# Optimization experiments

Measured on AMD Instinct MI355X. Metric: run time of the kernel, lower is better.

Reference implementation:

```python
import jax, jax.numpy as jnp
import numpy as np

NUM_CLASSES = 80
SCORE_THR = 0.2
NMS_THR = 0.3
MAX_PER_IMAGE = 100
TOPK_PER_CLASS = 100  # cap on pre-NMS candidates per (image, class); >= max_per_image
ANCHOR_MASK = [[6, 7, 8], [3, 4, 5], [0, 1, 2]]
COCO_ANCHORS = np.array([[10, 13], [16, 30], [33, 23], [30, 61], [62, 45],
                         [59, 119], [116, 90], [156, 198], [373, 326]], dtype=np.float32)


def yolo_head(feats, layer_anchors, num_classes, input_shape):
    # feats: [B, 3*(5+C), gh, gw]
    B = feats.shape[0]
    gh, gw = feats.shape[2], feats.shape[3]
    na = layer_anchors.shape[0]
    f = feats.reshape(B, na, num_classes + 5, gh, gw).transpose(0, 3, 4, 1, 2)  # [B,gh,gw,3,5+C]
    gy, gx = jnp.meshgrid(jnp.arange(gh), jnp.arange(gw), indexing='ij')
    grid = jnp.stack([gx, gy], axis=-1).astype(f.dtype)[None, :, :, None, :]  # [1,gh,gw,1,2]
    # literal translation: divide by tensor([gh, gw]) (square grids in practice)
    box_xy = (jax.nn.sigmoid(f[..., :2]) + grid) / jnp.array([gh, gw], f.dtype)
    box_wh = jnp.exp(f[..., 2:4]) * layer_anchors[None, None, None, :, :] / input_shape[None, None, None, None, :]
    conf = jax.nn.sigmoid(f[..., 4:5])
    probs = jax.nn.sigmoid(f[..., 5:])
    return box_xy, box_wh, conf, probs


def yolo_correct_boxes(box_xy, box_wh, input_shape, image_shape):
    box_yx = box_xy[..., ::-1]
    box_hw = box_wh[..., ::-1]
    new_shape = jnp.round(image_shape * jnp.min(input_shape / image_shape))
    offset = (input_shape - new_shape) / 2.0 / input_shape
    scale = input_shape / new_shape
    box_yx = (box_yx - offset) * scale
    box_hw = box_hw * scale
    mins = box_yx - box_hw / 2.0
    maxes = box_yx + box_hw / 2.0
    boxes = jnp.concatenate([mins, maxes], axis=-1)  # (ymin, xmin, ymax, xmax)
    return boxes * jnp.concatenate([image_shape, image_shape])


def decode_layer(feats, layer_anchors, input_shape, image_shape):
    box_xy, box_wh, conf, probs = yolo_head(feats, layer_anchors, NUM_CLASSES, input_shape)
    boxes = yolo_correct_boxes(box_xy, box_wh, input_shape, image_shape)  # [B,gh,gw,3,4]
    B = feats.shape[0]
    return boxes.reshape(B, -1, 4), (conf * probs).reshape(B, -1, NUM_CLASSES)


def pairwise_iou(b):
    # b: [K,4] (y1,x1,y2,x2)
    y1, x1, y2, x2 = b[:, 0], b[:, 1], b[:, 2], b[:, 3]
    area = jnp.maximum(y2 - y1, 0) * jnp.maximum(x2 - x1, 0)
    iy1 = jnp.maximum(y1[:, None], y1[None, :])
    ix1 = jnp.maximum(x1[:, None], x1[None, :])
    iy2 = jnp.minimum(y2[:, None], y2[None, :])
    ix2 = jnp.minimum(x2[:, None], x2[None, :])
    inter = jnp.maximum(iy2 - iy1, 0) * jnp.maximum(ix2 - ix1, 0)
    return inter / (area[:, None] + area[None, :] - inter + 1e-9)


def greedy_nms(boxes, valid):
    # boxes [K,4] sorted by descending score; valid [K] bool. Returns keep mask [K].
    K = boxes.shape[0]
    iou = jax.lax.stop_gradient(pairwise_iou(boxes))
    idx = jnp.arange(K)
    def body(i, sup):
        keep_i = valid[i] & (~sup[i])
        return sup | (keep_i & (iou[i] > NMS_THR) & (idx > i))
    sup = jax.lax.fori_loop(0, K, body, jnp.zeros((K,), bool))
    return valid & (~sup)


def setup_inputs() -> dict:
    key = jax.random.key(0)
    k0, k1, k2 = jax.random.split(key, 3)
    B, F = 16, 3 * (5 + NUM_CLASSES)
    feat0 = jax.random.normal(k0, (B, F, 19, 19), jnp.float32)
    feat1 = jax.random.normal(k1, (B, F, 38, 38), jnp.float32)
    feat2 = jax.random.normal(k2, (B, F, 76, 76), jnp.float32)
    anchors = jnp.asarray(COCO_ANCHORS)
    image_shape = jnp.array([480.0, 640.0], jnp.float32)
    return {"feat0": feat0, "feat1": feat1, "feat2": feat2,
            "anchors": anchors, "image_shape": image_shape}


def reference(feat0, feat1, feat2, anchors, image_shape):
    input_shape = jnp.array([feat0.shape[2] * 32, feat0.shape[3] * 32], jnp.float32)
    feats = [feat0, feat1, feat2]
    boxes_l, scores_l = [], []
    for l in range(3):
        b, s = decode_layer(feats[l], anchors[np.array(ANCHOR_MASK[l])], input_shape, image_shape)
        boxes_l.append(b)
        scores_l.append(s)
    boxes = jnp.concatenate(boxes_l, axis=1)    # [B,N,4]
    scores = jnp.concatenate(scores_l, axis=1)  # [B,N,C]
    B = scores.shape[0]
    sc = scores.transpose(0, 2, 1)              # [B,C,N]
    top_s, top_i = jax.lax.top_k(sc, TOPK_PER_CLASS)              # [B,C,K]
    top_b = jnp.take_along_axis(boxes[:, None, :, :], top_i[..., None], axis=2)  # [B,C,K,4]
    valid = top_s >= SCORE_THR
    keep = jax.vmap(jax.vmap(greedy_nms))(top_b, valid)           # [B,C,K]
    cand = jnp.where(keep, top_s, -1.0)
    flat_s = cand.reshape(B, -1)                 # [B, C*K]
    flat_b = top_b.reshape(B, -1, 4)
    sel_s, sel_i = jax.lax.top_k(flat_s, MAX_PER_IMAGE)           # [B,100]
    sel_b = jnp.take_along_axis(flat_b, sel_i[..., None], axis=1)  # [B,100,4]
    sel_c = (sel_i // TOPK_PER_CLASS).astype(jnp.float32)
    # dets: (ymin, xmin, ymax, xmax, score, class); score == -1 marks padding
    return jnp.concatenate([sel_b, sel_s[..., None], sel_c[..., None]], axis=-1)
```

## Files before the change

### kernel.cpp

```cpp
#include <hip/hip_runtime.h>
#include <hip/hip_bf16.h>


#define NTOT   22743
#define NCLS   80
#define TOPK   100
#define KPAD   22752
#define NVEC   2842
#define Q_L1   17328
#define Q_L0   21660
#define SCORE_THR 0.2f
#define NMS_THR   0.3f

__device__ __forceinline__ float sig_exact(float x) {
    return 1.0f / (1.0f + expf(-x));
}
__device__ __forceinline__ float sig_fast(float x) {
    return __builtin_amdgcn_rcpf(1.0f + __expf(-x));
}

__global__ __launch_bounds__(256) void k_decode(
    const float* __restrict__ f0, const float* __restrict__ f1,
    const float* __restrict__ f2, const float* __restrict__ anchors,
    const float* __restrict__ imshape, float4* __restrict__ boxes,
    float* __restrict__ conf_q, int total) {
    int gid = blockIdx.x * 256 + threadIdx.x;
    if (gid >= total) return;
    int b = gid / NTOT; int p = gid - b * NTOT;

    const float* f; int ghw, gw, l, off, a, s;
    if (p < 1083)      { f=f0; off=0;    ghw=361;  gw=19; l=0; int r=p;      a=r/361;  s=r-a*361;  }
    else if (p < 5415) { f=f1; off=1083; ghw=1444; gw=38; l=1; int r=p-1083; a=r/1444; s=r-a*1444; }
    else               { f=f2; off=5415; ghw=5776; gw=76; l=2; int r=p-5415; a=r/5776; s=r-a*5776; }
    int y = s / gw, x = s - y * gw;

    const float* q = f + ((size_t)(b * 255 + a * 85) * ghw + s);
    float tx = q[0], ty = q[ghw], tw = q[2*ghw], th = q[3*ghw], tc = q[4*ghw];

    int arow = (2 - l) * 3 + a;
    float aw = anchors[arow * 2], ah = anchors[arow * 2 + 1];
    float imh = imshape[0], imw = imshape[1];
    float gf = (float)gw;

    float bxx = (sig_exact(tx) + (float)x) / gf;
    float bxy = (sig_exact(ty) + (float)y) / gf;
    float bw  = expf(tw) * aw / 608.0f;
    float bh  = expf(th) * ah / 608.0f;

    float r  = fminf(608.0f / imh, 608.0f / imw);
    float nh = rintf(imh * r), nw = rintf(imw * r);
    float offy = (608.0f - nh) / 2.0f / 608.0f;
    float offx = (608.0f - nw) / 2.0f / 608.0f;
    float scy = 608.0f / nh, scx = 608.0f / nw;

    float cy = (bxy - offy) * scy;
    float cx = (bxx - offx) * scx;
    float hh = bh * scy, ww = bw * scx;

    int n = off + 3 * s + a;
    boxes[(size_t)b * NTOT + n] =
        make_float4((cy - hh / 2.0f) * imh, (cx - ww / 2.0f) * imw,
                    (cy + hh / 2.0f) * imh, (cx + ww / 2.0f) * imw);
    int qi = (l == 2) ? (a * 5776 + s)
           : (l == 1) ? (Q_L1 + a * 1444 + s)
                      : (Q_L0 + a * 361 + s);
    conf_q[(size_t)b * KPAD + qi] = sig_exact(tc);
}

#define SEG_A  346560
#define SEG_AB 433200
#define SEG_T  519840
__global__ __launch_bounds__(256) void k_score(
    const float* __restrict__ f0, const float* __restrict__ f1,
    const float* __restrict__ f2, const float* __restrict__ conf_q,
    unsigned short* __restrict__ keybuf, int total) {
    int gid = blockIdx.x * 256 + threadIdx.x;
    if (gid >= total) return;
    const int b = gid / SEG_T;
    const int w = gid - b * SEG_T;

    if (w < SEG_AB) {
        const float* f; int a, c, s, qbase, ghw;
        if (w < SEG_A) {
            a = w / 115520; int r = w - a * 115520;
            c = r / 1444;   s = (r - c * 1444) * 4;
            f = f2; ghw = 5776; qbase = a * 5776;
        } else {
            int t = w - SEG_A;
            a = t / 28880;  int r = t - a * 28880;
            c = r / 361;    s = (r - c * 361) * 4;
            f = f1; ghw = 1444; qbase = Q_L1 + a * 1444;
        }
        const float4 lg = *(const float4*)(f + ((size_t)(b * 255 + a * 85 + 5 + c) * ghw + s));
        const float4 cf = *(const float4*)(conf_q + (size_t)b * KPAD + qbase + s);
        ushort4 k;
        k.x = (unsigned short)(__float_as_uint(cf.x * sig_fast(lg.x)) >> 16);
        k.y = (unsigned short)(__float_as_uint(cf.y * sig_fast(lg.y)) >> 16);
        k.z = (unsigned short)(__float_as_uint(cf.z * sig_fast(lg.z)) >> 16);
        k.w = (unsigned short)(__float_as_uint(cf.w * sig_fast(lg.w)) >> 16);
        *(ushort4*)(keybuf + ((size_t)(b * NCLS + c)) * KPAD + qbase + s) = k;
    } else {
        int t = w - SEG_AB;
        int a = t / 28880;  int r = t - a * 28880;
        int c = r / 361;    int s = r - c * 361;
        int qi = Q_L0 + a * 361 + s;
        float lg = f0[((size_t)(b * 255 + a * 85 + 5 + c) * 361 + s)];
        float cf = conf_q[(size_t)b * KPAD + qi];
        keybuf[((size_t)(b * NCLS + c)) * KPAD + qi] =
            (unsigned short)(__float_as_uint(cf * sig_fast(lg)) >> 16);
    }
}

__device__ void find_pivot(unsigned* hist, int H, unsigned target,
                           unsigned* suf, unsigned* sh_p, unsigned* sh_above) {
    const int tid = threadIdx.x;
    const int per = H >> 8;
    if (tid < 256) {
        unsigned acc = 0;
        for (int u = 0; u < per; ++u) acc += hist[tid * per + u];
        suf[tid] = acc;
    }
    __syncthreads();
    for (int off = 1; off < 256; off <<= 1) {
        unsigned v = 0;
        if (tid < 256) v = (tid + off < 256) ? suf[tid + off] : 0u;
        __syncthreads();
        if (tid < 256) suf[tid] += v;
        __syncthreads();
    }
    if (tid < 256) {
        unsigned mysuf = suf[tid];
        unsigned nxt = (tid == 255) ? 0u : suf[tid + 1];
        if (mysuf >= target && nxt < target) {
            unsigned above = nxt;
            for (int h = tid * per + per - 1; h >= tid * per; --h) {
                unsigned c2 = above + hist[h];
                if (c2 >= target) { *sh_p = (unsigned)h; *sh_above = above; break; }
                above = c2;
            }
        }
    }
    __syncthreads();
}

__device__ __forceinline__ void collect_cand(
    int b, int c, int q, const float* __restrict__ f0,
    const float* __restrict__ f1, const float* __restrict__ f2,
    const float* __restrict__ conf_q, unsigned long long* buf,
    unsigned* sh_cnt) {
    int a, s, nbase, ghw;
    const float* f;
    if (q < Q_L1)      { a = q / 5776;  s = q - a * 5776;  f = f2; ghw = 5776; nbase = 5415; }
    else if (q < Q_L0) { int r = q - Q_L1; a = r / 1444; s = r - a * 1444; f = f1; ghw = 1444; nbase = 1083; }
    else               { int r = q - Q_L0; a = r / 361;  s = r - a * 361;  f = f0; ghw = 361;  nbase = 0;    }
    float t  = f[((size_t)(b * 255 + a * 85 + 5 + c)) * ghw + s];
    float cf = conf_q[(size_t)b * KPAD + q];
    float sce = cf * sig_exact(t);
    int n = nbase + 3 * s + a;
    unsigned slot = atomicAdd(sh_cnt, 1u);
    if (slot < 512)
        buf[slot] = (((unsigned long long)__float_as_uint(sce)) << 32)
                    | (unsigned)(~n);
}

__global__ __launch_bounds__(512, 8) void k_topk(
    const float* __restrict__ f0, const float* __restrict__ f1,
    const float* __restrict__ f2, const float* __restrict__ conf_q,
    const unsigned short* __restrict__ keybuf,
    const float4* __restrict__ boxes, float4* __restrict__ top_b,
    float* __restrict__ cand) {
    __shared__ unsigned int histp[4096];
    __shared__ unsigned long long buf[512];
    __shared__ unsigned int wsum[4];
    __shared__ float sb_y1[TOPK], sb_x1[TOPK], sb_y2[TOPK], sb_x2[TOPK], sb_s[TOPK];
    __shared__ unsigned int sh_p, sh_cnt;

    const int tid = threadIdx.x;
    const int row = blockIdx.x;
    const int b = row / NCLS, c = row - b * NCLS;
    const unsigned short* kr = keybuf + (size_t)row * KPAD;
    const uint4* kv = (const uint4*)kr;

    for (int i = tid; i < 4096; i += 512) histp[i] = 0;
    if (tid == 0) sh_cnt = 0;
    __syncthreads();

    uint4 v[6];
    bool  val[6];
    #pragma unroll
    for (int k = 0; k < 6; ++k) {
        int g = tid + k * 512;
        val[k] = (g < NVEC);
        v[k] = val[k] ? kv[g] : make_uint4(0, 0, 0, 0);
    }
    const bool hastail = (tid < NTOT - NVEC * 8);
    unsigned tailk = hastail ? (unsigned)kr[NVEC * 8 + tid] : 0u;

    #pragma unroll
    for (int k = 0; k < 6; ++k) if (val[k]) {
        unsigned ks[8] = { v[k].x & 0xFFFFu, v[k].x >> 16, v[k].y & 0xFFFFu, v[k].y >> 16,
                           v[k].z & 0xFFFFu, v[k].z >> 16, v[k].w & 0xFFFFu, v[k].w >> 16 };
        #pragma unroll
        for (int j = 0; j < 8; ++j)
            atomicAdd(&histp[ks[j] >> 2], 1u << (((ks[j] >> 1) & 1u) * 16));
    }
    if (hastail) atomicAdd(&histp[tailk >> 2], 1u << (((tailk >> 1) & 1u) * 16));
    __syncthreads();

    {
        const int lane = tid & 63;
        unsigned own = 0;
        if (tid < 256) {
            #pragma unroll
            for (int u = 0; u < 16; ++u) {
                unsigned w = histp[tid * 16 + u];
                own += (w & 0xFFFFu) + (w >> 16);
            }
        }
        unsigned acc = own;
        #pragma unroll
        for (int d = 1; d < 64; d <<= 1) {
            unsigned vv = __shfl_down(acc, d, 64);
            if (lane + d < 64) acc += vv;
        }
        if (tid < 256 && lane == 0) wsum[tid >> 6] = acc;
        __syncthreads();
        if (tid < 256) {
            unsigned tail = 0;
            for (int w2 = (tid >> 6) + 1; w2 < 4; ++w2) tail += wsum[w2];
            unsigned suft = acc + tail;
            unsigned nxt  = suft - own;
            if (suft >= TOPK && nxt < TOPK) {
                unsigned above = nxt;
                for (int bb = 31; bb >= 0; --bb) {
                    unsigned w = histp[tid * 16 + (bb >> 1)];
                    unsigned cnt = (bb & 1) ? (w >> 16) : (w & 0xFFFFu);
                    if (above + cnt >= TOPK) { sh_p = (unsigned)(tid * 32 + bb); break; }
                    above += cnt;
                }
            }
        }
        __syncthreads();
    }
    const unsigned kthr = sh_p > 0 ? ((sh_p - 1) << 1) : 0u;

    #pragma unroll
    for (int k = 0; k < 6; ++k) if (val[k]) {
        unsigned ks[8] = { v[k].x & 0xFFFFu, v[k].x >> 16, v[k].y & 0xFFFFu, v[k].y >> 16,
                           v[k].z & 0xFFFFu, v[k].z >> 16, v[k].w & 0xFFFFu, v[k].w >> 16 };
        #pragma unroll
        for (int j = 0; j < 8; ++j)
            if (ks[j] >= kthr)
                collect_cand(b, c, (tid + k * 512) * 8 + j, f0, f1, f2, conf_q, buf, &sh_cnt);
    }
    if (hastail && tailk >= kthr)
        collect_cand(b, c, NVEC * 8 + tid, f0, f1, f2, conf_q, buf, &sh_cnt);
    __syncthreads();

    const int M = (int)min(sh_cnt, 512u);
    if (tid < M) {
        unsigned long long mykey = buf[tid];
        int rank = 0;
        for (int j = 0; j < M; ++j) rank += (buf[j] > mykey);
        if (rank < TOPK) {
            int n = (int)(~(unsigned)mykey);
            float4 bx = boxes[(size_t)b * NTOT + n];
            sb_y1[rank] = bx.x; sb_x1[rank] = bx.y;
            sb_y2[rank] = bx.z; sb_x2[rank] = bx.w;
            sb_s[rank]  = __uint_as_float((unsigned)(mykey >> 32));
            top_b[(size_t)row * TOPK + rank] = bx;
        }
    }
    __syncthreads();

    if (tid < 64) {
        const int j0 = tid, j1 = tid + 64;
        const bool v1 = (j1 < TOPK);
        float y10 = sb_y1[j0], x10 = sb_x1[j0], y20 = sb_y2[j0], x20 = sb_x2[j0];
        float s0 = sb_s[j0];
        float y11 = v1 ? sb_y1[j1] : 0.f, x11 = v1 ? sb_x1[j1] : 0.f;
        float y21 = v1 ? sb_y2[j1] : 0.f, x21 = v1 ? sb_x2[j1] : 0.f;
        float s1 = v1 ? sb_s[j1] : -1.0f;
        float ar0 = fmaxf(y20 - y10, 0.f) * fmaxf(x20 - x10, 0.f);
        float ar1 = fmaxf(y21 - y11, 0.f) * fmaxf(x21 - x11, 0.f);
        int sup0 = 0, sup1 = 0;
        for (int i = 0; i < TOPK; ++i) {
            float yi1 = sb_y1[i], xi1 = sb_x1[i], yi2 = sb_y2[i], xi2 = sb_x2[i];
            float si = sb_s[i];
            int supi = (i < 64) ? __shfl(sup0, i, 64) : __shfl(sup1, i - 64, 64);
            bool keep_i = (si >= SCORE_THR) && (supi == 0);
            if (keep_i) {
                float ari = fmaxf(yi2 - yi1, 0.f) * fmaxf(xi2 - xi1, 0.f);
                if (j0 > i) {
                    float ty1 = fmaxf(yi1, y10), tx1 = fmaxf(xi1, x10);
                    float ty2 = fminf(yi2, y20), tx2 = fminf(xi2, x20);
                    float inter = fmaxf(ty2 - ty1, 0.f) * fmaxf(tx2 - tx1, 0.f);
                    float iou = inter / (ari + ar0 - inter + 1e-9f);
                    if (iou > NMS_THR) sup0 = 1;
                }
                if (v1 && j1 > i) {
                    float ty1 = fmaxf(yi1, y11), tx1 = fmaxf(xi1, x11);
                    float ty2 = fminf(yi2, y21), tx2 = fminf(xi2, x21);
                    float inter = fmaxf(ty2 - ty1, 0.f) * fmaxf(tx2 - tx1, 0.f);
                    float iou = inter / (ari + ar1 - inter + 1e-9f);
                    if (iou > NMS_THR) sup1 = 1;
                }
            }
        }
        cand[(size_t)row * TOPK + j0] = (s0 >= SCORE_THR && sup0 == 0) ? s0 : -1.0f;
        if (v1)
            cand[(size_t)row * TOPK + j1] = (s1 >= SCORE_THR && sup1 == 0) ? s1 : -1.0f;
    }
}

__global__ __launch_bounds__(256) void k_final(
    const float* __restrict__ cand, const float4* __restrict__ top_b,
    float* __restrict__ out) {
    __shared__ float cs[8000];
    __shared__ unsigned int hist[4096];
    __shared__ unsigned long long buf[512];
    __shared__ unsigned int suf[256];
    __shared__ unsigned int sh_kp, sh_p1, sh_above1, sh_p2, sh_above2, sh_cnt;

    const int tid = threadIdx.x, b = blockIdx.x;
    if (tid == 0) { sh_kp = 0; sh_cnt = 0; }
    for (int i = tid; i < 4096; i += 256) hist[i] = 0;
    __syncthreads();

    unsigned lk = 0;
    for (int i = tid; i < 8000; i += 256) {
        float v = cand[b * 8000 + i];
        cs[i] = v;
        if (v > -0.5f) lk++;
    }
    atomicAdd(&sh_kp, lk);
    __syncthreads();
    unsigned Kp = sh_kp;

    if (Kp >= TOPK) {
        for (int i = tid; i < 8000; i += 256)
            if (cs[i] > -0.5f) atomicAdd(&hist[__float_as_uint(cs[i]) >> 19], 1u);
        __syncthreads();
        find_pivot(hist, 2048, TOPK, suf, &sh_p1, &sh_above1);
        unsigned p1 = sh_p1, above1 = sh_above1;
        for (int i = tid; i < 4096; i += 256) hist[i] = 0;
        __syncthreads();
        for (int i = tid; i < 8000; i += 256) {
            float v = cs[i];
            if (v > -0.5f) {
                unsigned bits = __float_as_uint(v);
                if ((bits >> 19) == p1) atomicAdd(&hist[(bits >> 7) & 0xFFFu], 1u);
            }
        }
        __syncthreads();
        find_pivot(hist, 4096, TOPK - above1, suf, &sh_p2, &sh_above2);
        unsigned p2 = sh_p2;
        for (int i = tid; i < 8000; i += 256) {
            float v = cs[i];
            if (v > -0.5f) {
                unsigned bits = __float_as_uint(v);
                unsigned b1 = bits >> 19;
                if (b1 > p1 || (b1 == p1 && ((bits >> 7) & 0xFFFu) >= p2)) {
                    unsigned slot = atomicAdd(&sh_cnt, 1u);
                    if (slot < 512)
                        buf[slot] = (((unsigned long long)bits) << 32) | (unsigned)(~i);
                }
            }
        }
    } else {
        for (int i = tid; i < 8000; i += 256) {
            float v = cs[i];
            if (v > -0.5f) {
                unsigned slot = atomicAdd(&sh_cnt, 1u);
                buf[slot] = (((unsigned long long)__float_as_uint(v)) << 32) | (unsigned)(~i);
            }
        }
        __syncthreads();
        if (tid == 0) {
            unsigned need = TOPK - Kp, got = 0;
            for (int i = 0; i < 8000 && got < need; ++i)
                if (cs[i] <= -0.5f) { buf[Kp + got] = (unsigned)(~i); got++; }
        }
    }
    __syncthreads();

    const int M2 = (Kp >= TOPK) ? (int)min(sh_cnt, 512u) : (int)TOPK;
    for (int i = tid; i < M2; i += 256) {
        unsigned long long key = buf[i];
        int rank = 0;
        for (int j = 0; j < M2; ++j) rank += (buf[j] > key);
        if (rank < TOPK) {
            int fi = (int)(~(unsigned)key);
            int c = fi / TOPK; int kk = fi - c * TOPK;
            float4 bb = top_b[((size_t)b * NCLS + c) * TOPK + kk];
            int base = (b * TOPK + rank) * 6;
            out[base + 0] = bb.x; out[base + 1] = bb.y;
            out[base + 2] = bb.z; out[base + 3] = bb.w;
            out[base + 4] = cs[fi]; out[base + 5] = (float)c;
        }
    }
}

extern "C" void kernel_launch(void* const* d_in, const int* in_sizes, int n_in,
                              void* d_out, int out_size, void* d_ws, size_t ws_size,
                              hipStream_t stream) {
    (void)n_in; (void)out_size; (void)ws_size;
    const float* f0      = (const float*)d_in[0];
    const float* f1      = (const float*)d_in[1];
    const float* f2      = (const float*)d_in[2];
    const float* anchors = (const float*)d_in[3];
    const float* imshape = (const float*)d_in[4];
    const int B = in_sizes[0] / (255 * 19 * 19);

    char* ws = (char*)d_ws;
    size_t o = 0;
    unsigned short* keybuf = (unsigned short*)(ws + o);
    o += (size_t)B * NCLS * KPAD * sizeof(unsigned short);
    float4* boxes  = (float4*)(ws + o); o += (size_t)B * NTOT * sizeof(float4);
    float*  conf_q = (float*)(ws + o);  o += (size_t)B * KPAD * sizeof(float);
    float4* top_b  = (float4*)(ws + o); o += (size_t)B * NCLS * TOPK * sizeof(float4);
    float*  cand   = (float*)(ws + o);  o += (size_t)B * NCLS * TOPK * sizeof(float);
    float*  out    = (float*)d_out;

    const int total = B * NTOT;
    k_decode<<<(total + 255) / 256, 256, 0, stream>>>(f0, f1, f2, anchors, imshape,
                                                      boxes, conf_q, total);
    const int stotal = B * SEG_T;
    k_score<<<(stotal + 255) / 256, 256, 0, stream>>>(f0, f1, f2, conf_q,
                                                      keybuf, stotal);
    k_topk<<<B * NCLS, 512, 0, stream>>>(f0, f1, f2, conf_q, keybuf, boxes,
                                         top_b, cand);
    k_final<<<B, 256, 0, stream>>>(cand, top_b, out);
}
```

Measured before the change: 265.1 us.

## Fuse score computation into top-k kernel, dropping the 16-bit key buffer

```diff
diff --git a/kernel.cpp b/kernel.cpp
--- a/kernel.cpp
+++ b/kernel.cpp
@@ -7,6 +7,7 @@
 #define TOPK   100
 #define KPAD   22752
 #define NVEC   2842
+#define NVEC2  2166
 #define Q_L1   17328
 #define Q_L0   21660
 #define SCORE_THR 0.2f
@@ -65,50 +66,6 @@
            : (l == 1) ? (Q_L1 + a * 1444 + s)
                       : (Q_L0 + a * 361 + s);
     conf_q[(size_t)b * KPAD + qi] = sig_exact(tc);
-}
-
-#define SEG_A  346560
-#define SEG_AB 433200
-#define SEG_T  519840
-__global__ __launch_bounds__(256) void k_score(
-    const float* __restrict__ f0, const float* __restrict__ f1,
-    const float* __restrict__ f2, const float* __restrict__ conf_q,
-    unsigned short* __restrict__ keybuf, int total) {
-    int gid = blockIdx.x * 256 + threadIdx.x;
-    if (gid >= total) return;
-    const int b = gid / SEG_T;
-    const int w = gid - b * SEG_T;
-
-    if (w < SEG_AB) {
-        const float* f; int a, c, s, qbase, ghw;
-        if (w < SEG_A) {
-            a = w / 115520; int r = w - a * 115520;
-            c = r / 1444;   s = (r - c * 1444) * 4;
-            f = f2; ghw = 5776; qbase = a * 5776;
-        } else {
-            int t = w - SEG_A;
-            a = t / 28880;  int r = t - a * 28880;
-            c = r / 361;    s = (r - c * 361) * 4;
-            f = f1; ghw = 1444; qbase = Q_L1 + a * 1444;
-        }
-        const float4 lg = *(const float4*)(f + ((size_t)(b * 255 + a * 85 + 5 + c) * ghw + s));
-        const float4 cf = *(const float4*)(conf_q + (size_t)b * KPAD + qbase + s);
-        ushort4 k;
-        k.x = (unsigned short)(__float_as_uint(cf.x * sig_fast(lg.x)) >> 16);
-        k.y = (unsigned short)(__float_as_uint(cf.y * sig_fast(lg.y)) >> 16);
-        k.z = (unsigned short)(__float_as_uint(cf.z * sig_fast(lg.z)) >> 16);
-        k.w = (unsigned short)(__float_as_uint(cf.w * sig_fast(lg.w)) >> 16);
-        *(ushort4*)(keybuf + ((size_t)(b * NCLS + c)) * KPAD + qbase + s) = k;
-    } else {
-        int t = w - SEG_AB;
-        int a = t / 28880;  int r = t - a * 28880;
-        int c = r / 361;    int s = r - c * 361;
-        int qi = Q_L0 + a * 361 + s;
-        float lg = f0[((size_t)(b * 255 + a * 85 + 5 + c) * 361 + s)];
-        float cf = conf_q[(size_t)b * KPAD + qi];
-        keybuf[((size_t)(b * NCLS + c)) * KPAD + qi] =
-            (unsigned short)(__float_as_uint(cf * sig_fast(lg)) >> 16);
-    }
 }
 
 __device__ void find_pivot(unsigned* hist, int H, unsigned target,
@@ -141,6 +98,22 @@
         }
     }
     __syncthreads();
+}
+
+__device__ __forceinline__ float load_logit(int b, int c, int q,
+    const float* __restrict__ f0, const float* __restrict__ f1,
+    const float* __restrict__ f2) {
+    int a, s, ghw; const float* f;
+    if (q < Q_L1)      { f = f2; ghw = 5776; a = q / 5776;  s = q - a * 5776; }
+    else if (q < Q_L0) { f = f1; ghw = 1444; int r = q - Q_L1; a = r / 1444; s = r - a * 1444; }
+    else               { f = f0; ghw = 361;  int r = q - Q_L0; a = r / 361;  s = r - a * 361; }
+    return f[((size_t)(b * 255 + a * 85 + 5 + c)) * ghw + s];
+}
+
+__device__ __forceinline__ unsigned pack2(float cfa, float lga, float cfb, float lgb) {
+    unsigned ka = __float_as_uint(cfa * sig_fast(lga)) >> 16;
+    unsigned kb = __float_as_uint(cfb * sig_fast(lgb)) >> 16;
+    return ka | (kb << 16);
 }
 
 __device__ __forceinline__ void collect_cand(
@@ -166,7 +139,6 @@
 __global__ __launch_bounds__(512, 8) void k_topk(
     const float* __restrict__ f0, const float* __restrict__ f1,
     const float* __restrict__ f2, const float* __restrict__ conf_q,
-    const unsigned short* __restrict__ keybuf,
     const float4* __restrict__ boxes, float4* __restrict__ top_b,
     float* __restrict__ cand) {
     __shared__ unsigned int histp[4096];
@@ -178,12 +150,10 @@
     const int tid = threadIdx.x;
     const int row = blockIdx.x;
     const int b = row / NCLS, c = row - b * NCLS;
-    const unsigned short* kr = keybuf + (size_t)row * KPAD;
-    const uint4* kv = (const uint4*)kr;
+    const float* cq = conf_q + (size_t)b * KPAD;
 
     for (int i = tid; i < 4096; i += 512) histp[i] = 0;
     if (tid == 0) sh_cnt = 0;
-    __syncthreads();
 
     uint4 v[6];
     bool  val[6];
@@ -191,10 +161,37 @@
     for (int k = 0; k < 6; ++k) {
         int g = tid + k * 512;
         val[k] = (g < NVEC);
-        v[k] = val[k] ? kv[g] : make_uint4(0, 0, 0, 0);
+        if (val[k]) {
+            int q = g * 8;
+            if (g < NVEC2) {
+                int a = q / 5776, s = q - a * 5776;
+                const float* fp = f2 + ((size_t)(b * 255 + a * 85 + 5 + c)) * 5776 + s;
+                float4 l0 = *(const float4*)fp;
+                float4 l1 = *(const float4*)(fp + 4);
+                float4 c0 = *(const float4*)(cq + q);
+                float4 c1 = *(const float4*)(cq + q + 4);
+                v[k].x = pack2(c0.x, l0.x, c0.y, l0.y);
+                v[k].y = pack2(c0.z, l0.z, c0.w, l0.w);
+                v[k].z = pack2(c1.x, l1.x, c1.y, l1.y);
+                v[k].w = pack2(c1.z, l1.z, c1.w, l1.w);
+            } else {
+                float lg[8];
+                #pragma unroll
+                for (int j = 0; j < 8; ++j) lg[j] = load_logit(b, c, q + j, f0, f1, f2);
+                v[k].x = pack2(cq[q + 0], lg[0], cq[q + 1], lg[1]);
+                v[k].y = pack2(cq[q + 2], lg[2], cq[q + 3], lg[3]);
+                v[k].z = pack2(cq[q + 4], lg[4], cq[q + 5], lg[5]);
+                v[k].w = pack2(cq[q + 6], lg[6], cq[q + 7], lg[7]);
+            }
+        } else v[k] = make_uint4(0, 0, 0, 0);
     }
     const bool hastail = (tid < NTOT - NVEC * 8);
-    unsigned tailk = hastail ? (unsigned)kr[NVEC * 8 + tid] : 0u;
+    unsigned tailk = 0;
+    if (hastail) {
+        int q = NVEC * 8 + tid;
+        tailk = __float_as_uint(cq[q] * sig_fast(load_logit(b, c, q, f0, f1, f2))) >> 16;
+    }
+    __syncthreads();
 
     #pragma unroll
     for (int k = 0; k < 6; ++k) if (val[k]) {
@@ -414,8 +411,6 @@
 
     char* ws = (char*)d_ws;
     size_t o = 0;
-    unsigned short* keybuf = (unsigned short*)(ws + o);
-    o += (size_t)B * NCLS * KPAD * sizeof(unsigned short);
     float4* boxes  = (float4*)(ws + o); o += (size_t)B * NTOT * sizeof(float4);
     float*  conf_q = (float*)(ws + o);  o += (size_t)B * KPAD * sizeof(float);
     float4* top_b  = (float4*)(ws + o); o += (size_t)B * NCLS * TOPK * sizeof(float4);
@@ -425,10 +420,7 @@
     const int total = B * NTOT;
     k_decode<<<(total + 255) / 256, 256, 0, stream>>>(f0, f1, f2, anchors, imshape,
                                                       boxes, conf_q, total);
-    const int stotal = B * SEG_T;
-    k_score<<<(stotal + 255) / 256, 256, 0, stream>>>(f0, f1, f2, conf_q,
-                                                      keybuf, stotal);
-    k_topk<<<B * NCLS, 512, 0, stream>>>(f0, f1, f2, conf_q, keybuf, boxes,
+    k_topk<<<B * NCLS, 512, 0, stream>>>(f0, f1, f2, conf_q, boxes,
                                          top_b, cand);
     k_final<<<B, 256, 0, stream>>>(cand, top_b, out);
 }
```

Measured after the change: 278.7 us. +5.1%, slower.

## Fuse score computation into decode kernel and shrink top-k blocks to 256 threads

Applied to the files above, without the earlier changes.

```diff
diff --git a/kernel.cpp b/kernel.cpp
--- a/kernel.cpp
+++ b/kernel.cpp
@@ -19,11 +19,12 @@
     return __builtin_amdgcn_rcpf(1.0f + __expf(-x));
 }
 
-__global__ __launch_bounds__(256) void k_decode(
+__global__ __launch_bounds__(256) void k_decode_score(
     const float* __restrict__ f0, const float* __restrict__ f1,
     const float* __restrict__ f2, const float* __restrict__ anchors,
     const float* __restrict__ imshape, float4* __restrict__ boxes,
-    float* __restrict__ conf_q, int total) {
+    float* __restrict__ conf_q, unsigned short* __restrict__ keybuf,
+    int total) {
     int gid = blockIdx.x * 256 + threadIdx.x;
     if (gid >= total) return;
     int b = gid / NTOT; int p = gid - b * NTOT;
@@ -61,52 +62,19 @@
     boxes[(size_t)b * NTOT + n] =
         make_float4((cy - hh / 2.0f) * imh, (cx - ww / 2.0f) * imw,
                     (cy + hh / 2.0f) * imh, (cx + ww / 2.0f) * imw);
+
     int qi = (l == 2) ? (a * 5776 + s)
            : (l == 1) ? (Q_L1 + a * 1444 + s)
                       : (Q_L0 + a * 361 + s);
-    conf_q[(size_t)b * KPAD + qi] = sig_exact(tc);
-}
-
-#define SEG_A  346560
-#define SEG_AB 433200
-#define SEG_T  519840
-__global__ __launch_bounds__(256) void k_score(
-    const float* __restrict__ f0, const float* __restrict__ f1,
-    const float* __restrict__ f2, const float* __restrict__ conf_q,
-    unsigned short* __restrict__ keybuf, int total) {
-    int gid = blockIdx.x * 256 + threadIdx.x;
-    if (gid >= total) return;
-    const int b = gid / SEG_T;
-    const int w = gid - b * SEG_T;
-
-    if (w < SEG_AB) {
-        const float* f; int a, c, s, qbase, ghw;
-        if (w < SEG_A) {
-            a = w / 115520; int r = w - a * 115520;
-            c = r / 1444;   s = (r - c * 1444) * 4;
-            f = f2; ghw = 5776; qbase = a * 5776;
-        } else {
-            int t = w - SEG_A;
-            a = t / 28880;  int r = t - a * 28880;
-            c = r / 361;    s = (r - c * 361) * 4;
-            f = f1; ghw = 1444; qbase = Q_L1 + a * 1444;
-        }
-        const float4 lg = *(const float4*)(f + ((size_t)(b * 255 + a * 85 + 5 + c) * ghw + s));
-        const float4 cf = *(const float4*)(conf_q + (size_t)b * KPAD + qbase + s);
-        ushort4 k;
-        k.x = (unsigned short)(__float_as_uint(cf.x * sig_fast(lg.x)) >> 16);
-        k.y = (unsigned short)(__float_as_uint(cf.y * sig_fast(lg.y)) >> 16);
-        k.z = (unsigned short)(__float_as_uint(cf.z * sig_fast(lg.z)) >> 16);
-        k.w = (unsigned short)(__float_as_uint(cf.w * sig_fast(lg.w)) >> 16);
-        *(ushort4*)(keybuf + ((size_t)(b * NCLS + c)) * KPAD + qbase + s) = k;
-    } else {
-        int t = w - SEG_AB;
-        int a = t / 28880;  int r = t - a * 28880;
-        int c = r / 361;    int s = r - c * 361;
-        int qi = Q_L0 + a * 361 + s;
-        float lg = f0[((size_t)(b * 255 + a * 85 + 5 + c) * 361 + s)];
-        float cf = conf_q[(size_t)b * KPAD + qi];
-        keybuf[((size_t)(b * NCLS + c)) * KPAD + qi] =
+    float cf = sig_exact(tc);
+    conf_q[(size_t)b * KPAD + qi] = cf;
+
+    const float* lp = f + ((size_t)(b * 255 + a * 85 + 5) * ghw + s);
+    unsigned short* kb = keybuf + (size_t)b * NCLS * KPAD + qi;
+    #pragma unroll 4
+    for (int c = 0; c < NCLS; ++c) {
+        float lg = lp[(size_t)c * ghw];
+        kb[(size_t)c * KPAD] =
             (unsigned short)(__float_as_uint(cf * sig_fast(lg)) >> 16);
     }
 }
@@ -163,7 +131,7 @@
                     | (unsigned)(~n);
 }
 
-__global__ __launch_bounds__(512, 8) void k_topk(
+__global__ __launch_bounds__(256, 5) void k_topk(
     const float* __restrict__ f0, const float* __restrict__ f1,
     const float* __restrict__ f2, const float* __restrict__ conf_q,
     const unsigned short* __restrict__ keybuf,
@@ -181,23 +149,23 @@
     const unsigned short* kr = keybuf + (size_t)row * KPAD;
     const uint4* kv = (const uint4*)kr;
 
-    for (int i = tid; i < 4096; i += 512) histp[i] = 0;
+    for (int i = tid; i < 4096; i += 256) histp[i] = 0;
     if (tid == 0) sh_cnt = 0;
-    __syncthreads();
-
-    uint4 v[6];
-    bool  val[6];
+
+    uint4 v[12];
+    bool  val[12];
     #pragma unroll
-    for (int k = 0; k < 6; ++k) {
-        int g = tid + k * 512;
+    for (int k = 0; k < 12; ++k) {
+        int g = tid + k * 256;
         val[k] = (g < NVEC);
         v[k] = val[k] ? kv[g] : make_uint4(0, 0, 0, 0);
     }
     const bool hastail = (tid < NTOT - NVEC * 8);
     unsigned tailk = hastail ? (unsigned)kr[NVEC * 8 + tid] : 0u;
+    __syncthreads();
 
     #pragma unroll
-    for (int k = 0; k < 6; ++k) if (val[k]) {
+    for (int k = 0; k < 12; ++k) if (val[k]) {
         unsigned ks[8] = { v[k].x & 0xFFFFu, v[k].x >> 16, v[k].y & 0xFFFFu, v[k].y >> 16,
                            v[k].z & 0xFFFFu, v[k].z >> 16, v[k].w & 0xFFFFu, v[k].w >> 16 };
         #pragma unroll
@@ -210,12 +178,10 @@
     {
         const int lane = tid & 63;
         unsigned own = 0;
-        if (tid < 256) {
-            #pragma unroll
-            for (int u = 0; u < 16; ++u) {
-                unsigned w = histp[tid * 16 + u];
-                own += (w & 0xFFFFu) + (w >> 16);
-            }
+        #pragma unroll
+        for (int u = 0; u < 16; ++u) {
+            unsigned w = histp[tid * 16 + u];
+            own += (w & 0xFFFFu) + (w >> 16);
         }
         unsigned acc = own;
         #pragma unroll
@@ -223,9 +189,9 @@
             unsigned vv = __shfl_down(acc, d, 64);
             if (lane + d < 64) acc += vv;
         }
-        if (tid < 256 && lane == 0) wsum[tid >> 6] = acc;
-        __syncthreads();
-        if (tid < 256) {
+        if (lane == 0) wsum[tid >> 6] = acc;
+        __syncthreads();
+        {
             unsigned tail = 0;
             for (int w2 = (tid >> 6) + 1; w2 < 4; ++w2) tail += wsum[w2];
             unsigned suft = acc + tail;
@@ -245,21 +211,21 @@
     const unsigned kthr = sh_p > 0 ? ((sh_p - 1) << 1) : 0u;
 
     #pragma unroll
-    for (int k = 0; k < 6; ++k) if (val[k]) {
+    for (int k = 0; k < 12; ++k) if (val[k]) {
         unsigned ks[8] = { v[k].x & 0xFFFFu, v[k].x >> 16, v[k].y & 0xFFFFu, v[k].y >> 16,
                            v[k].z & 0xFFFFu, v[k].z >> 16, v[k].w & 0xFFFFu, v[k].w >> 16 };
         #pragma unroll
         for (int j = 0; j < 8; ++j)
             if (ks[j] >= kthr)
-                collect_cand(b, c, (tid + k * 512) * 8 + j, f0, f1, f2, conf_q, buf, &sh_cnt);
+                collect_cand(b, c, (tid + k * 256) * 8 + j, f0, f1, f2, conf_q, buf, &sh_cnt);
     }
     if (hastail && tailk >= kthr)
         collect_cand(b, c, NVEC * 8 + tid, f0, f1, f2, conf_q, buf, &sh_cnt);
     __syncthreads();
 
     const int M = (int)min(sh_cnt, 512u);
-    if (tid < M) {
-        unsigned long long mykey = buf[tid];
+    for (int i = tid; i < M; i += 256) {
+        unsigned long long mykey = buf[i];
         int rank = 0;
         for (int j = 0; j < M; ++j) rank += (buf[j] > mykey);
         if (rank < TOPK) {
@@ -423,12 +389,9 @@
     float*  out    = (float*)d_out;
 
     const int total = B * NTOT;
-    k_decode<<<(total + 255) / 256, 256, 0, stream>>>(f0, f1, f2, anchors, imshape,
-                                                      boxes, conf_q, total);
-    const int stotal = B * SEG_T;
-    k_score<<<(stotal + 255) / 256, 256, 0, stream>>>(f0, f1, f2, conf_q,
-                                                      keybuf, stotal);
-    k_topk<<<B * NCLS, 512, 0, stream>>>(f0, f1, f2, conf_q, keybuf, boxes,
+    k_decode_score<<<(total + 255) / 256, 256, 0, stream>>>(
+        f0, f1, f2, anchors, imshape, boxes, conf_q, keybuf, total);
+    k_topk<<<B * NCLS, 256, 0, stream>>>(f0, f1, f2, conf_q, keybuf, boxes,
                                          top_b, cand);
     k_final<<<B, 256, 0, stream>>>(cand, top_b, out);
 }
```

Result: slower. 276.1 us (+4.2%).
